# Kernel optimization log

Hardware: AMD Instinct MI355X
Metric: run time of the kernel (lower is better)

## Reference

```python
import jax, jax.numpy as jnp
from jax import lax
import numpy as np

B, N, DIM = 2, 2048, 1024
HEADS, DIM_HEAD = 16, 64
KERNELS = (0, 3, 5, 7)
GROUPS = len(KERNELS)
HPG = HEADS // GROUPS          # heads per group = 4
CG = HPG * DIM_HEAD            # channels per group for depthwise conv = 256
INNER = HEADS * DIM_HEAD       # 1024


def _alibi_slopes(n):
    # power-of-2 branch of LearnedAlibiPosBias._get_slopes (n=4 here)
    start = 2.0 ** (-(2.0 ** -(np.log2(n) - 3)))
    return np.array([start * start ** i for i in range(n)], dtype=np.float32)


def setup_inputs() -> dict:
    key = jax.random.key(0)
    ks = jax.random.split(key, 24)
    d = {}
    d['x'] = jax.random.normal(ks[0], (B, N, DIM), jnp.float32)
    d['ln_gamma'] = jnp.ones((DIM,), jnp.float32)
    d['ln_beta'] = jnp.zeros((DIM,), jnp.float32)
    d['w_qkv'] = jax.random.normal(ks[1], (3 * INNER, DIM), jnp.float32) * 0.02
    i = 2
    for p in ('q', 'k', 'v'):
        for ksz in (3, 5, 7):
            d[f'dw{p}_w{ksz}'] = jax.random.normal(ks[i], (CG, 1, ksz), jnp.float32) * 0.1; i += 1
            d[f'dw{p}_b{ksz}'] = jax.random.normal(ks[i], (CG,), jnp.float32) * 0.02; i += 1
    # learned alibi slopes, initialized to the standard ALiBi values per group
    sl = _alibi_slopes(HPG).reshape(1, HPG, 1, 1)
    d['slopes'] = jnp.asarray(np.tile(sl, (GROUPS, 1, 1, 1)))
    d['w_out'] = jax.random.normal(ks[20], (DIM, INNER), jnp.float32) * 0.02
    return d


def _dw_causal_conv(xg, w, b, ksz):
    # xg: (B, CG, N); depthwise causal conv, left pad ksz-1
    xg = jnp.pad(xg, ((0, 0), (0, 0), (ksz - 1, 0)))
    out = lax.conv_general_dilated(xg, w, (1,), 'VALID',
                                   feature_group_count=CG,
                                   dimension_numbers=('NCH', 'OIH', 'NCH'))
    return out + b[None, :, None]


def _grouped_conv(t, w3, b3, w5, b5, w7, b7):
    # t: (B, INNER, N) channels laid out head-major; group g = channels [g*CG,(g+1)*CG)
    parts = [t[:, :CG]]  # group 0: kernel_size 0 -> Identity
    for i, (w, b, ksz) in enumerate(((w3, b3, 3), (w5, b5, 5), (w7, b7, 7))):
        parts.append(_dw_causal_conv(t[:, (i + 1) * CG:(i + 2) * CG], w, b, ksz))
    out = jnp.concatenate(parts, axis=1)                      # (B, INNER, N)
    out = out.reshape(B, HEADS, DIM_HEAD, N)
    return jnp.transpose(out, (0, 1, 3, 2))                   # (B, H, N, Dh)


def _forward(x, ln_gamma, ln_beta, w_qkv,
             dwq_w3, dwq_b3, dwq_w5, dwq_b5, dwq_w7, dwq_b7,
             dwk_w3, dwk_b3, dwk_w5, dwk_b5, dwk_w7, dwk_b7,
             dwv_w3, dwv_b3, dwv_w5, dwv_b5, dwv_w7, dwv_b7,
             slopes, w_out):
    scale = DIM_HEAD ** -0.5
    mu = jnp.mean(x, axis=-1, keepdims=True)
    var = jnp.var(x, axis=-1, keepdims=True)
    h = (x - mu) * lax.rsqrt(var + 1e-5) * ln_gamma + ln_beta   # (B, N, DIM)
    qkv = jnp.einsum('bnd,ed->ben', h, w_qkv)                   # (B, 3*INNER, N)
    q, k, v = jnp.split(qkv, 3, axis=1)
    q = _grouped_conv(q, dwq_w3, dwq_b3, dwq_w5, dwq_b5, dwq_w7, dwq_b7)
    k = _grouped_conv(k, dwk_w3, dwk_b3, dwk_w5, dwk_b5, dwk_w7, dwk_b7)
    v = _grouped_conv(v, dwv_w3, dwv_b3, dwv_w5, dwv_b5, dwv_w7, dwv_b7)
    sim = jnp.einsum('bhid,bhjd->bhij', q * scale, k)           # (B, H, N, N)
    idx = jnp.arange(N)
    dist = -jnp.abs(idx[None, :] - idx[:, None]).astype(sim.dtype)  # (N, N)
    bias = slopes.reshape(HEADS, 1, 1) * dist[None]             # (H, N, N)
    sim = sim + bias[None]
    causal = idx[None, :] > idx[:, None]                        # strictly future
    sim = jnp.where(causal[None, None], -jnp.finfo(sim.dtype).max, sim)
    attn = jax.nn.softmax(sim, axis=-1)
    out = jnp.einsum('bhij,bhjd->bhid', attn, v)                # (B, H, N, Dh)
    out = jnp.transpose(out, (0, 2, 1, 3)).reshape(B, N, INNER)
    return jnp.einsum('bne,de->bnd', out, w_out)


def reference(x, ln_gamma, ln_beta, w_qkv,
              dwq_w3, dwq_b3, dwq_w5, dwq_b5, dwq_w7, dwq_b7,
              dwk_w3, dwk_b3, dwk_w5, dwk_b5, dwk_w7, dwk_b7,
              dwv_w3, dwv_b3, dwv_w5, dwv_b5, dwv_w7, dwv_b7,
              slopes, w_out):
    return _forward(x, ln_gamma, ln_beta, w_qkv,
                    dwq_w3, dwq_b3, dwq_w5, dwq_b5, dwq_w7, dwq_b7,
                    dwk_w3, dwk_b3, dwk_w5, dwk_b5, dwk_w7, dwk_b7,
                    dwv_w3, dwv_b3, dwv_w5, dwv_b5, dwv_w7, dwv_b7,
                    slopes, w_out)
```

## Files before the change

### kernel.cpp

```cpp
#include <hip/hip_runtime.h>
#include <hip/hip_bf16.h>
#include <stdint.h>

typedef __bf16 bf8 __attribute__((ext_vector_type(8)));
typedef float  f4  __attribute__((ext_vector_type(4)));

constexpr int BATCH  = 2;
constexpr int SEQ    = 2048;
constexpr int DMODEL = 1024;
constexpr int NH     = 16;
constexpr int DHEAD  = 64;
constexpr int E3     = 3072;

static __device__ __forceinline__ f4 mfma16(bf8 a, bf8 b, f4 c){
  return __builtin_amdgcn_mfma_f32_16x16x32_bf16(a, b, c, 0, 0, 0);
}
static __device__ __forceinline__ uint32_t pack2(float a, float b){
  union { __bf16 h[2]; uint32_t u; } p;
  p.h[0] = (__bf16)a; p.h[1] = (__bf16)b;
  return p.u;
}
typedef const __attribute__((address_space(1))) uint32_t g_u32;
typedef __attribute__((address_space(3))) uint32_t l_u32;
static __device__ __forceinline__ void glds16(const __bf16* g, __bf16* l){
  __builtin_amdgcn_global_load_lds((g_u32*)g, (l_u32*)l, 16, 0, 0);
}

__global__ __launch_bounds__(256) void prep_kernel(const float* __restrict__ x,
                                                   const float* __restrict__ gam,
                                                   const float* __restrict__ bet,
                                                   __bf16* __restrict__ h,
                                                   const float* __restrict__ wq,
                                                   __bf16* __restrict__ wqb){
  int bid = blockIdx.x;
  int tid = threadIdx.x;
  if(bid >= BATCH*SEQ){
    int i = ((bid - BATCH*SEQ) * 256 + tid) * 4;
    float4 v = *(const float4*)(wq + i);
    __bf16 o[4] = {(__bf16)v.x, (__bf16)v.y, (__bf16)v.z, (__bf16)v.w};
    *(uint2*)(wqb + i) = *(const uint2*)o;
    return;
  }
  int row = bid;
  const float* xr = x + (size_t)row * DMODEL;
  float4 v = *(const float4*)(xr + tid*4);
  float s = v.x + v.y + v.z + v.w;
  float ss = v.x*v.x + v.y*v.y + v.z*v.z + v.w*v.w;
#pragma unroll
  for(int m=1;m<64;m<<=1){ s += __shfl_xor(s, m); ss += __shfl_xor(ss, m); }
  __shared__ float sm[8];
  int wid = tid >> 6;
  if((tid & 63) == 0){ sm[wid] = s; sm[4+wid] = ss; }
  __syncthreads();
  s  = sm[0]+sm[1]+sm[2]+sm[3];
  ss = sm[4]+sm[5]+sm[6]+sm[7];
  float mu  = s * (1.f/DMODEL);
  float var = ss * (1.f/DMODEL) - mu*mu;
  float r = rsqrtf(var + 1e-5f);
  float4 g = *(const float4*)(gam + tid*4);
  float4 bb = *(const float4*)(bet + tid*4);
  __bf16 o[4] = { (__bf16)((v.x-mu)*r*g.x + bb.x), (__bf16)((v.y-mu)*r*g.y + bb.y),
                  (__bf16)((v.z-mu)*r*g.z + bb.z), (__bf16)((v.w-mu)*r*g.w + bb.w) };
  *(uint2*)(h + (size_t)row*DMODEL + tid*4) = *(uint2*)o;
}

template<typename CT>
__global__ __launch_bounds__(256) void gemm_nt(const __bf16* __restrict__ A,
                                               const __bf16* __restrict__ Bm,
                                               CT* __restrict__ C,
                                               int M, int Ncols, int K){
  __shared__ __align__(16) __bf16 smem[4*128*32];
  __bf16* As0 = smem;
  __bf16* Bs0 = smem + 2*128*32;
  int m0 = blockIdx.y * 128, n0 = blockIdx.x * 128;
  int tid = threadIdx.x;
  int lane = tid & 63, wid = tid >> 6;
  int quad = lane >> 4, l15 = lane & 15;
  int wm = (wid >> 1) * 64, wn = (wid & 1) * 64;
  f4 acc[4][4] = {};
  int r0 = wid*32 + (lane >> 2);
  int cofs = (lane & 3) * 8;
  const __bf16* ag = A  + (size_t)(m0 + r0) * K + cofs;
  const __bf16* bg = Bm + (size_t)(n0 + r0) * K + cofs;
  const int d0 = (wid*32)*32, d1 = (wid*32+16)*32;
  const size_t rowskip = (size_t)16 * K;
  glds16(ag,           As0 + d0);
  glds16(ag + rowskip, As0 + d1);
  glds16(bg,           Bs0 + d0);
  glds16(bg + rowskip, Bs0 + d1);
  __syncthreads();
  int cur = 0;
  for(int k0 = 0; k0 < K; k0 += 32){
    int k1 = k0 + 32;
    if(k1 < K){
      int nb = cur ^ 1;
      glds16(ag + k1,           As0 + nb*128*32 + d0);
      glds16(ag + rowskip + k1, As0 + nb*128*32 + d1);
      glds16(bg + k1,           Bs0 + nb*128*32 + d0);
      glds16(bg + rowskip + k1, Bs0 + nb*128*32 + d1);
    }
    const __bf16* AsC = As0 + cur*128*32;
    const __bf16* BsC = Bs0 + cur*128*32;
    bf8 af[4], bfr[4];
#pragma unroll
    for(int i=0;i<4;i++){
      af[i]  = *(const bf8*)&AsC[(wm + i*16 + l15)*32 + quad*8];
      bfr[i] = *(const bf8*)&BsC[(wn + i*16 + l15)*32 + quad*8];
    }
#pragma unroll
    for(int mi=0;mi<4;mi++)
#pragma unroll
      for(int ni=0;ni<4;ni++)
        acc[mi][ni] = mfma16(af[mi], bfr[ni], acc[mi][ni]);
    __syncthreads();
    cur ^= 1;
  }
  if constexpr (sizeof(CT) == 2){
    __bf16* scr = smem;
    uint32_t* sp = (uint32_t*)smem;
#pragma unroll
    for(int qq=0; qq<4; qq++){
      __syncthreads();
      if((wid>>1) == (qq>>1)){
        int mi0 = (qq & 1) * 2;
#pragma unroll
        for(int mm=0; mm<2; mm++){
          int mi = mi0 + mm;
#pragma unroll
          for(int ni=0; ni<4; ni++)
#pragma unroll
            for(int r=0; r<4; r++){
              int lr = (mi - mi0)*16 + quad*4 + r;
              scr[lr*136 + wn + ni*16 + l15] = (__bf16)acc[mi][ni][r];
            }
        }
      }
      __syncthreads();
#pragma unroll
      for(int it=0; it<2; it++){
        int idx = it*256 + tid;
        int row = idx >> 4;
        int ck  = idx & 15;
        uint4 v = { sp[row*68 + ck*4 + 0], sp[row*68 + ck*4 + 1],
                    sp[row*68 + ck*4 + 2], sp[row*68 + ck*4 + 3] };
        *(uint4*)(C + (size_t)(m0 + qq*32 + row)*Ncols + n0 + ck*8) = v;
      }
    }
  } else {
    float* scr = (float*)smem;
#pragma unroll
    for(int qq=0; qq<4; qq++){
      __syncthreads();
      if((wid>>1) == (qq>>1)){
        int mi0 = (qq & 1) * 2;
#pragma unroll
        for(int mm=0; mm<2; mm++){
          int mi = mi0 + mm;
#pragma unroll
          for(int ni=0; ni<4; ni++)
#pragma unroll
            for(int r=0; r<4; r++){
              int lr = (mi - mi0)*16 + quad*4 + r;
              scr[lr*136 + wn + ni*16 + l15] = acc[mi][ni][r];
            }
        }
      }
      __syncthreads();
#pragma unroll
      for(int it=0; it<4; it++){
        int idx = it*256 + tid;
        int row = idx >> 5;
        int ck  = idx & 31;
        float4 v = { scr[row*136 + ck*4 + 0], scr[row*136 + ck*4 + 1],
                     scr[row*136 + ck*4 + 2], scr[row*136 + ck*4 + 3] };
        *(float4*)(C + (size_t)(m0 + qq*32 + row)*Ncols + n0 + ck*4) = v;
      }
    }
  }
}

__global__ __launch_bounds__(256) void conv_kernel(const __bf16* __restrict__ qkv,
    __bf16* __restrict__ qo, __bf16* __restrict__ ko, __bf16* __restrict__ vt,
    const float* qw3,const float* qb3,const float* qw5,const float* qb5,const float* qw7,const float* qb7,
    const float* kw3,const float* kb3,const float* kw5,const float* kb5,const float* kw7,const float* kb7,
    const float* vw3,const float* vb3,const float* vw5,const float* vb5,const float* vw7,const float* vb7){
  __shared__ __align__(16) __bf16 tile[72*256];
  int nc = blockIdx.x;
  int ec = blockIdx.y;
  int b  = blockIdx.z;
  int tid = threadIdx.x;
  int n0 = nc * 64;
  {
    int rrow = tid >> 5;
    int ccol = (tid & 31) * 8;
    const __bf16* src = qkv + (size_t)b*SEQ*E3 + ec*256 + ccol;
#pragma unroll
    for(int p=0;p<9;p++){
      int row = p*8 + rrow;
      int n = n0 - 8 + row;
      uint4 v = {0u,0u,0u,0u};
      if(n >= 0) v = *(const uint4*)(src + (size_t)n*E3);
      *(uint4*)&tile[row*256 + ccol] = v;
    }
  }
  __syncthreads();
  int e = ec*256 + tid;
  int p  = e >> 10;
  int c  = e & 1023;
  int g  = c >> 8;
  int cg = c & 255;
  int hh = c >> 6;
  int dh = c & 63;
  const float* W[9]  = {qw3,qw5,qw7,kw3,kw5,kw7,vw3,vw5,vw7};
  const float* Bp[9] = {qb3,qb5,qb7,kb3,kb5,kb7,vb3,vb5,vb7};
  int ksz = (g==0)?0:((g==1)?3:((g==2)?5:7));
  float w[7] = {0,0,0,0,0,0,0};
  float bias = 0.f;
  if(g > 0){
    const float* wp = W[p*3 + g - 1];
    const float* bp = Bp[p*3 + g - 1];
    for(int t=0;t<ksz;t++) w[t] = wp[cg*ksz + t];
    bias = bp[cg];
  }
  float xh[6];
#pragma unroll
  for(int i=0;i<6;i++) xh[i] = (float)tile[(2+i)*256 + tid];
  if(p == 2){
    uint32_t vout[32];
#pragma unroll
    for(int blk=0; blk<8; blk++){
      __bf16 tmp[8];
#pragma unroll
      for(int u=0;u<8;u++){
        int dn = blk*8 + u;
        float cur = (float)tile[(8+dn)*256 + tid];
        float o;
        if(ksz == 0)      o = cur;
        else if(ksz == 3) o = w[0]*xh[4] + w[1]*xh[5] + w[2]*cur + bias;
        else if(ksz == 5) o = w[0]*xh[2] + w[1]*xh[3] + w[2]*xh[4] + w[3]*xh[5] + w[4]*cur + bias;
        else              o = w[0]*xh[0] + w[1]*xh[1] + w[2]*xh[2] + w[3]*xh[3] + w[4]*xh[4] + w[5]*xh[5] + w[6]*cur + bias;
        xh[0]=xh[1]; xh[1]=xh[2]; xh[2]=xh[3]; xh[3]=xh[4]; xh[4]=xh[5]; xh[5]=cur;
        tmp[u] = (__bf16)o;
      }
#pragma unroll
      for(int j=0;j<4;j++) vout[blk*4 + j] = ((const uint32_t*)tmp)[j];
    }
    __syncthreads();
    uint32_t* ot = (uint32_t*)tile;
#pragma unroll
    for(int j=0;j<32;j++) ot[tid*33 + j] = vout[j];
    __syncthreads();
#pragma unroll
    for(int it=0; it<8; it++){
      int idx = it*256 + tid;
      int ch  = idx >> 3;
      int ncq = idx & 7;
      uint32_t a0 = ot[ch*33 + ncq*4 + 0];
      uint32_t a1 = ot[ch*33 + ncq*4 + 1];
      uint32_t a2 = ot[ch*33 + ncq*4 + 2];
      uint32_t a3 = ot[ch*33 + ncq*4 + 3];
      uint4 val = {a0, a1, a2, a3};
      int hh2 = (ec & 3)*4 + (ch >> 6);
      int dh2 = ch & 63;
      *(uint4*)(vt + ((size_t)((b*NH + hh2)*DHEAD + dh2))*SEQ + n0 + ncq*8) = val;
    }
  } else {
    __bf16* outp = (p==0) ? qo : ko;
    __bf16* op = outp + ((size_t)(b*NH + hh)*SEQ)*DHEAD + dh;
#pragma unroll 4
    for(int dn=0; dn<64; dn++){
      float cur = (float)tile[(8+dn)*256 + tid];
      float o;
      if(ksz == 0)      o = cur;
      else if(ksz == 3) o = w[0]*xh[4] + w[1]*xh[5] + w[2]*cur + bias;
      else if(ksz == 5) o = w[0]*xh[2] + w[1]*xh[3] + w[2]*xh[4] + w[3]*xh[5] + w[4]*cur + bias;
      else              o = w[0]*xh[0] + w[1]*xh[1] + w[2]*xh[2] + w[3]*xh[3] + w[4]*xh[4] + w[5]*xh[5] + w[6]*cur + bias;
      xh[0]=xh[1]; xh[1]=xh[2]; xh[2]=xh[3]; xh[3]=xh[4]; xh[4]=xh[5]; xh[5]=cur;
      op[(size_t)(n0+dn)*DHEAD] = (__bf16)o;
    }
  }
}

__global__ __launch_bounds__(256, 2) void attn_kernel(const __bf16* __restrict__ Qin,
                                                      const __bf16* __restrict__ Kin,
                                                      const __bf16* __restrict__ Vtin,
                                                      const float* __restrict__ slopes,
                                                      __bf16* __restrict__ Oout,
                                                      const float* __restrict__ wsrc,
                                                      __bf16* __restrict__ wdst){
  __shared__ __align__(16) __bf16 Ks[2][128*64];
  __shared__ __align__(16) __bf16 Vts[2][64*128];
  __shared__ __align__(16) __bf16 Ps[4][16*72];
  __shared__ float Al[4][16];
  int bid = blockIdx.x;
  int tid = threadIdx.x;
  if(bid >= 512){
    int i = ((bid - 512) * 256 + tid) * 4;
    float4 v = *(const float4*)(wsrc + i);
    __bf16 o[4] = {(__bf16)v.x, (__bf16)v.y, (__bf16)v.z, (__bf16)v.w};
    *(uint2*)(wdst + i) = *(const uint2*)o;
    return;
  }
  int pr = bid >> 5;
  int by = (bid & 7) + ((bid >> 3) & 3) * 8;
  int b  = by >> 4, hh = by & 15;
  int lane = tid & 63, w = tid >> 6;
  int quad = lane >> 4, l15 = lane & 15;
  const __bf16* qb  = Qin  + (size_t)by * SEQ * DHEAD;
  const __bf16* kb  = Kin  + (size_t)by * SEQ * DHEAD;
  const __bf16* vtb = Vtin + (size_t)by * DHEAD * SEQ;
  const float L2E = 1.4426950408889634f;
  float slope = slopes[hh];
  const float c1 = 0.125f * L2E;
  float c2 = slope * L2E;
  float c2_64 = c2 * 64.f;
  float cjb[16];
#pragma unroll
  for(int jt=0;jt<4;jt++)
#pragma unroll
    for(int r=0;r<4;r++)
      cjb[jt*4+r] = c2 * (float)(jt*16 + quad*4 + r);

  int sxq0 = ((quad     ^ (l15 & 7)) << 3);
  int sxq1 = (((quad+4) ^ (l15 & 7)) << 3);

  const __bf16* ksrc = kb + (size_t)(lane>>3)*DHEAD + ((lane&7) ^ ((lane>>3)&7))*8;
  const __bf16* vsrc[4];
#pragma unroll
  for(int u=0;u<4;u++){
    int g = w*4 + u;
    int vrow = g*4 + (lane>>4);
    vsrc[u] = vtb + (size_t)vrow*SEQ + (((lane&15) ^ (vrow&15)) * 8);
  }

  for(int ph=0; ph<2; ph++){
    int qi = ph ? (31 - pr) : pr;
    int q0 = qi * 64;
    int nst = (qi >> 1) + 1;
    int i0 = q0 + w*16;
    int i  = i0 + l15;
    bf8 aq0 = *(const bf8*)(qb + (size_t)i*DHEAD + quad*8);
    bf8 aq1 = *(const bf8*)(qb + (size_t)i*DHEAD + 32 + quad*8);
    f4 oacc[4] = {};
    float l_ = 0.f;
#pragma unroll
    for(int u=0;u<4;u++){
      int g = w*4 + u;
      glds16(ksrc + (size_t)g*8*DHEAD, &Ks[0][g*512]);
      glds16(vsrc[u],                  &Vts[0][g*512]);
    }
    __syncthreads();
    int cur = 0;
    for(int t=0; t<nst; t++){
      int j0 = t*128;
      bool pf = (t+1) < nst;
      if(pf){
        int nb = cur ^ 1;
#pragma unroll
        for(int u=0;u<4;u++){
          int g = w*4 + u;
          glds16(ksrc + (size_t)((t+1)*128 + g*8)*DHEAD, &Ks[nb][g*512]);
          glds16(vsrc[u] + (t+1)*128,                    &Vts[nb][g*512]);
        }
      }
      const __bf16* KsC  = Ks[cur];
      const __bf16* VtsC = Vts[cur];
      f4 s[8] = {};
      __builtin_amdgcn_s_setprio(1);
#pragma unroll
      for(int jt=0;jt<8;jt++){
        bf8 ak0 = *(const bf8*)&KsC[(jt*16+l15)*64 + sxq0];
        bf8 ak1 = *(const bf8*)&KsC[(jt*16+l15)*64 + sxq1];
        s[jt] = mfma16(ak0, aq0, s[jt]);
        s[jt] = mfma16(ak1, aq1, s[jt]);
      }
      __builtin_amdgcn_s_setprio(0);
      float lsum = 0.f;
      bool masked = (t == nst-1);
      float cdi = c2 * (float)(i - j0) + 8.0f;
#pragma unroll
      for(int h=0;h<2;h++){
        bf8 bv[2][4];
#pragma unroll
        for(int jj=0;jj<2;jj++){
          int jk = h*2 + jj;
#pragma unroll
          for(int nd=0;nd<4;nd++)
            bv[jj][nd] = *(const bf8*)&VtsC[(nd*16+l15)*128 + (((jk*4+quad) ^ l15) << 3)];
        }
        float sv[4][4];
        if(!masked){
#pragma unroll
          for(int jl=0;jl<4;jl++){
            int jt = h*4 + jl;
#pragma unroll
            for(int r=0;r<4;r++)
              sv[jl][r] = fmaf(s[jt][r], c1, cjb[jl*4+r] - cdi + (h ? c2_64 : 0.f));
          }
        } else {
#pragma unroll
          for(int jl=0;jl<4;jl++){
            int jt = h*4 + jl;
#pragma unroll
            for(int r=0;r<4;r++){
              int j = j0 + jt*16 + quad*4 + r;
              int d = i - j;
              float val = fmaf(s[jt][r], c1, -fmaf(c2, (float)d, 8.0f));
              sv[jl][r] = (d < 0) ? -1e30f : val;
            }
          }
        }
#pragma unroll
        for(int jl=0;jl<4;jl++){
          float p0 = __builtin_amdgcn_exp2f(sv[jl][0]);
          float p1 = __builtin_amdgcn_exp2f(sv[jl][1]);
          float p2 = __builtin_amdgcn_exp2f(sv[jl][2]);
          float p3 = __builtin_amdgcn_exp2f(sv[jl][3]);
          lsum += (p0+p1)+(p2+p3);
          uint2 pk = { pack2(p0,p1), pack2(p2,p3) };
          *(uint2*)&Ps[w][l15*72 + jl*16 + quad*4] = pk;
        }
        __builtin_amdgcn_s_setprio(1);
#pragma unroll
        for(int jj=0;jj<2;jj++){
          bf8 ap = *(const bf8*)&Ps[w][l15*72 + jj*32 + quad*8];
#pragma unroll
          for(int nd=0;nd<4;nd++)
            oacc[nd] = mfma16(ap, bv[jj][nd], oacc[nd]);
        }
        __builtin_amdgcn_s_setprio(0);
      }
      lsum += __shfl_xor(lsum, 16);
      lsum += __shfl_xor(lsum, 32);
      l_ += lsum;
      __syncthreads();
      cur ^= 1;
    }
    if(quad == 0) Al[w][l15] = 1.0f / l_;
    f4 linv = *(const f4*)&Al[w][quad*4];
#pragma unroll
    for(int nd=0;nd<4;nd++)
#pragma unroll
      for(int r=0;r<4;r++){
        int io = i0 + quad*4 + r;
        Oout[((size_t)(b*SEQ + io))*DMODEL + hh*64 + nd*16 + l15] =
            (__bf16)(oacc[nd][r] * linv[r]);
      }
    if(ph == 0) __syncthreads();
  }
}

extern "C" void kernel_launch(void* const* d_in, const int* in_sizes, int n_in,
                              void* d_out, int out_size, void* d_ws, size_t ws_size,
                              hipStream_t stream){
  const float* x      = (const float*)d_in[0];
  const float* gam    = (const float*)d_in[1];
  const float* bet    = (const float*)d_in[2];
  const float* w_qkv  = (const float*)d_in[3];
  const float* slopes = (const float*)d_in[22];
  const float* w_out  = (const float*)d_in[23];
  float* out = (float*)d_out;

  char* ws = (char*)d_ws;
  __bf16* h       = (__bf16*)(ws);
  __bf16* qpost   = (__bf16*)(ws);
  __bf16* qkv     = (__bf16*)(ws + ((size_t)8  << 20));
  __bf16* att     = (__bf16*)(ws + ((size_t)8  << 20));
  __bf16* wout_bf = (__bf16*)(ws + ((size_t)24 << 20));
  __bf16* wqkv_bf = (__bf16*)(ws + ((size_t)32 << 20));
  __bf16* kpost   = (__bf16*)(ws + ((size_t)32 << 20));
  __bf16* vtp     = (__bf16*)(ws + ((size_t)40 << 20));

  constexpr int NQKV = 3 * DMODEL * DMODEL;

  prep_kernel<<<BATCH*SEQ + NQKV/4/256, 256, 0, stream>>>(x, gam, bet, h, w_qkv, wqkv_bf);
  gemm_nt<__bf16><<<dim3(E3/128, (BATCH*SEQ)/128), 256, 0, stream>>>(
      h, wqkv_bf, qkv, BATCH*SEQ, E3, DMODEL);
  conv_kernel<<<dim3(32, 12, BATCH), 256, 0, stream>>>(qkv, qpost, kpost, vtp,
    (const float*)d_in[4],(const float*)d_in[5],(const float*)d_in[6],(const float*)d_in[7],
    (const float*)d_in[8],(const float*)d_in[9],
    (const float*)d_in[10],(const float*)d_in[11],(const float*)d_in[12],(const float*)d_in[13],
    (const float*)d_in[14],(const float*)d_in[15],
    (const float*)d_in[16],(const float*)d_in[17],(const float*)d_in[18],(const float*)d_in[19],
    (const float*)d_in[20],(const float*)d_in[21]);
  attn_kernel<<<dim3(1536), 256, 0, stream>>>(qpost, kpost, vtp, slopes, att,
                                              w_out, wout_bf);
  gemm_nt<float><<<dim3(DMODEL/128, (BATCH*SEQ)/128), 256, 0, stream>>>(
      att, wout_bf, out, BATCH*SEQ, DMODEL, DMODEL);
}
```

Before: 235.5 us.

## Split attention into one q-tile per block with 64-wide KV tiles

The attention kernel now gives each block a single 64-row query tile, processed longest first, instead of pairing a short and a long tile inside one block. The grid grows from 512 to 1024 attention blocks. KV tiles shrink from 128 to 64 columns, which halves shared memory and raises launch bounds to 3 blocks per CU for better occupancy and finer causal load balance. In exchange there are more loop iterations and barriers per key, and blocks now finish unevenly rather than being balanced by the pairing.

```diff
diff --git a/kernel.cpp b/kernel.cpp
--- a/kernel.cpp
+++ b/kernel.cpp
@@ -281,27 +281,27 @@
   }
 }
 
-__global__ __launch_bounds__(256, 2) void attn_kernel(const __bf16* __restrict__ Qin,
+__global__ __launch_bounds__(256, 3) void attn_kernel(const __bf16* __restrict__ Qin,
                                                       const __bf16* __restrict__ Kin,
                                                       const __bf16* __restrict__ Vtin,
                                                       const float* __restrict__ slopes,
                                                       __bf16* __restrict__ Oout,
                                                       const float* __restrict__ wsrc,
                                                       __bf16* __restrict__ wdst){
-  __shared__ __align__(16) __bf16 Ks[2][128*64];
-  __shared__ __align__(16) __bf16 Vts[2][64*128];
+  __shared__ __align__(16) __bf16 Ks[2][64*64];
+  __shared__ __align__(16) __bf16 Vts[2][64*64];
   __shared__ __align__(16) __bf16 Ps[4][16*72];
   __shared__ float Al[4][16];
   int bid = blockIdx.x;
   int tid = threadIdx.x;
-  if(bid >= 512){
-    int i = ((bid - 512) * 256 + tid) * 4;
+  if(bid >= 1024){
+    int i = ((bid - 1024) * 256 + tid) * 4;
     float4 v = *(const float4*)(wsrc + i);
     __bf16 o[4] = {(__bf16)v.x, (__bf16)v.y, (__bf16)v.z, (__bf16)v.w};
     *(uint2*)(wdst + i) = *(const uint2*)o;
     return;
   }
-  int pr = bid >> 5;
+  int qi = 31 - (bid >> 5);
   int by = (bid & 7) + ((bid >> 3) & 3) * 8;
   int b  = by >> 4, hh = by & 15;
   int lane = tid & 63, w = tid >> 6;
@@ -313,7 +313,6 @@
   float slope = slopes[hh];
   const float c1 = 0.125f * L2E;
   float c2 = slope * L2E;
-  float c2_64 = c2 * 64.f;
   float cjb[16];
 #pragma unroll
   for(int jt=0;jt<4;jt++)
@@ -324,130 +323,113 @@
   int sxq0 = ((quad     ^ (l15 & 7)) << 3);
   int sxq1 = (((quad+4) ^ (l15 & 7)) << 3);
 
-  const __bf16* ksrc = kb + (size_t)(lane>>3)*DHEAD + ((lane&7) ^ ((lane>>3)&7))*8;
-  const __bf16* vsrc[4];
-#pragma unroll
-  for(int u=0;u<4;u++){
-    int g = w*4 + u;
-    int vrow = g*4 + (lane>>4);
-    vsrc[u] = vtb + (size_t)vrow*SEQ + (((lane&15) ^ (vrow&15)) * 8);
-  }
-
-  for(int ph=0; ph<2; ph++){
-    int qi = ph ? (31 - pr) : pr;
-    int q0 = qi * 64;
-    int nst = (qi >> 1) + 1;
-    int i0 = q0 + w*16;
-    int i  = i0 + l15;
-    bf8 aq0 = *(const bf8*)(qb + (size_t)i*DHEAD + quad*8);
-    bf8 aq1 = *(const bf8*)(qb + (size_t)i*DHEAD + 32 + quad*8);
-    f4 oacc[4] = {};
-    float l_ = 0.f;
-#pragma unroll
-    for(int u=0;u<4;u++){
-      int g = w*4 + u;
-      glds16(ksrc + (size_t)g*8*DHEAD, &Ks[0][g*512]);
-      glds16(vsrc[u],                  &Vts[0][g*512]);
-    }
+  int r8 = lane >> 3;
+  int c8 = lane & 7;
+  int sw = (c8 ^ r8) * 8;
+  const __bf16* ksrc = kb  + (size_t)r8*DHEAD + sw;
+  const __bf16* vsrc = vtb + (size_t)r8*SEQ  + sw;
+  int g0 = w*2, g1 = w*2 + 1;
+  const size_t kg0o = (size_t)g0*8*DHEAD, kg1o = (size_t)g1*8*DHEAD;
+  const size_t vg0o = (size_t)g0*8*SEQ,   vg1o = (size_t)g1*8*SEQ;
+
+  int q0 = qi * 64;
+  int nst = qi + 1;
+  int i0 = q0 + w*16;
+  int i  = i0 + l15;
+  bf8 aq0 = *(const bf8*)(qb + (size_t)i*DHEAD + quad*8);
+  bf8 aq1 = *(const bf8*)(qb + (size_t)i*DHEAD + 32 + quad*8);
+  f4 oacc[4] = {};
+  float l_ = 0.f;
+  glds16(ksrc + kg0o, &Ks[0][g0*512]);
+  glds16(ksrc + kg1o, &Ks[0][g1*512]);
+  glds16(vsrc + vg0o, &Vts[0][g0*512]);
+  glds16(vsrc + vg1o, &Vts[0][g1*512]);
+  __syncthreads();
+  int cur = 0;
+  for(int t=0; t<nst; t++){
+    int j0 = t*64;
+    bool pf = (t+1) < nst;
+    if(pf){
+      int nb = cur ^ 1;
+      size_t off = (size_t)(t+1)*64;
+      glds16(ksrc + off*DHEAD + kg0o, &Ks[nb][g0*512]);
+      glds16(ksrc + off*DHEAD + kg1o, &Ks[nb][g1*512]);
+      glds16(vsrc + vg0o + off,       &Vts[nb][g0*512]);
+      glds16(vsrc + vg1o + off,       &Vts[nb][g1*512]);
+    }
+    const __bf16* KsC  = Ks[cur];
+    const __bf16* VtsC = Vts[cur];
+    f4 s[4] = {};
+    __builtin_amdgcn_s_setprio(1);
+#pragma unroll
+    for(int jt=0;jt<4;jt++){
+      bf8 ak0 = *(const bf8*)&KsC[(jt*16+l15)*64 + sxq0];
+      bf8 ak1 = *(const bf8*)&KsC[(jt*16+l15)*64 + sxq1];
+      s[jt] = mfma16(ak0, aq0, s[jt]);
+      s[jt] = mfma16(ak1, aq1, s[jt]);
+    }
+    __builtin_amdgcn_s_setprio(0);
+    bf8 bv[2][4];
+#pragma unroll
+    for(int jk=0;jk<2;jk++)
+#pragma unroll
+      for(int nd=0;nd<4;nd++)
+        bv[jk][nd] = *(const bf8*)&VtsC[(nd*16+l15)*64 + (((jk*4+quad) ^ (l15&7)) << 3)];
+    float sv[4][4];
+    if(t < nst-1){
+      float cdi = c2 * (float)(i - j0) + 8.0f;
+#pragma unroll
+      for(int jt=0;jt<4;jt++)
+#pragma unroll
+        for(int r=0;r<4;r++)
+          sv[jt][r] = fmaf(s[jt][r], c1, cjb[jt*4+r] - cdi);
+    } else {
+#pragma unroll
+      for(int jt=0;jt<4;jt++)
+#pragma unroll
+        for(int r=0;r<4;r++){
+          int j = j0 + jt*16 + quad*4 + r;
+          int d = i - j;
+          float val = fmaf(s[jt][r], c1, -fmaf(c2, (float)d, 8.0f));
+          sv[jt][r] = (d < 0) ? -1e30f : val;
+        }
+    }
+    float lsum = 0.f;
+#pragma unroll
+    for(int jt=0;jt<4;jt++){
+      float p0 = __builtin_amdgcn_exp2f(sv[jt][0]);
+      float p1 = __builtin_amdgcn_exp2f(sv[jt][1]);
+      float p2 = __builtin_amdgcn_exp2f(sv[jt][2]);
+      float p3 = __builtin_amdgcn_exp2f(sv[jt][3]);
+      lsum += (p0+p1)+(p2+p3);
+      uint2 pk = { pack2(p0,p1), pack2(p2,p3) };
+      *(uint2*)&Ps[w][l15*72 + jt*16 + quad*4] = pk;
+    }
+    lsum += __shfl_xor(lsum, 16);
+    lsum += __shfl_xor(lsum, 32);
+    l_ += lsum;
+    __builtin_amdgcn_s_setprio(1);
+#pragma unroll
+    for(int jk=0;jk<2;jk++){
+      bf8 ap = *(const bf8*)&Ps[w][l15*72 + jk*32 + quad*8];
+#pragma unroll
+      for(int nd=0;nd<4;nd++)
+        oacc[nd] = mfma16(ap, bv[jk][nd], oacc[nd]);
+    }
+    __builtin_amdgcn_s_setprio(0);
     __syncthreads();
-    int cur = 0;
-    for(int t=0; t<nst; t++){
-      int j0 = t*128;
-      bool pf = (t+1) < nst;
-      if(pf){
-        int nb = cur ^ 1;
-#pragma unroll
-        for(int u=0;u<4;u++){
-          int g = w*4 + u;
-          glds16(ksrc + (size_t)((t+1)*128 + g*8)*DHEAD, &Ks[nb][g*512]);
-          glds16(vsrc[u] + (t+1)*128,                    &Vts[nb][g*512]);
-        }
-      }
-      const __bf16* KsC  = Ks[cur];
-      const __bf16* VtsC = Vts[cur];
-      f4 s[8] = {};
-      __builtin_amdgcn_s_setprio(1);
-#pragma unroll
-      for(int jt=0;jt<8;jt++){
-        bf8 ak0 = *(const bf8*)&KsC[(jt*16+l15)*64 + sxq0];
-        bf8 ak1 = *(const bf8*)&KsC[(jt*16+l15)*64 + sxq1];
-        s[jt] = mfma16(ak0, aq0, s[jt]);
-        s[jt] = mfma16(ak1, aq1, s[jt]);
-      }
-      __builtin_amdgcn_s_setprio(0);
-      float lsum = 0.f;
-      bool masked = (t == nst-1);
-      float cdi = c2 * (float)(i - j0) + 8.0f;
-#pragma unroll
-      for(int h=0;h<2;h++){
-        bf8 bv[2][4];
-#pragma unroll
-        for(int jj=0;jj<2;jj++){
-          int jk = h*2 + jj;
-#pragma unroll
-          for(int nd=0;nd<4;nd++)
-            bv[jj][nd] = *(const bf8*)&VtsC[(nd*16+l15)*128 + (((jk*4+quad) ^ l15) << 3)];
-        }
-        float sv[4][4];
-        if(!masked){
-#pragma unroll
-          for(int jl=0;jl<4;jl++){
-            int jt = h*4 + jl;
-#pragma unroll
-            for(int r=0;r<4;r++)
-              sv[jl][r] = fmaf(s[jt][r], c1, cjb[jl*4+r] - cdi + (h ? c2_64 : 0.f));
-          }
-        } else {
-#pragma unroll
-          for(int jl=0;jl<4;jl++){
-            int jt = h*4 + jl;
-#pragma unroll
-            for(int r=0;r<4;r++){
-              int j = j0 + jt*16 + quad*4 + r;
-              int d = i - j;
-              float val = fmaf(s[jt][r], c1, -fmaf(c2, (float)d, 8.0f));
-              sv[jl][r] = (d < 0) ? -1e30f : val;
-            }
-          }
-        }
-#pragma unroll
-        for(int jl=0;jl<4;jl++){
-          float p0 = __builtin_amdgcn_exp2f(sv[jl][0]);
-          float p1 = __builtin_amdgcn_exp2f(sv[jl][1]);
-          float p2 = __builtin_amdgcn_exp2f(sv[jl][2]);
-          float p3 = __builtin_amdgcn_exp2f(sv[jl][3]);
-          lsum += (p0+p1)+(p2+p3);
-          uint2 pk = { pack2(p0,p1), pack2(p2,p3) };
-          *(uint2*)&Ps[w][l15*72 + jl*16 + quad*4] = pk;
-        }
-        __builtin_amdgcn_s_setprio(1);
-#pragma unroll
-        for(int jj=0;jj<2;jj++){
-          bf8 ap = *(const bf8*)&Ps[w][l15*72 + jj*32 + quad*8];
-#pragma unroll
-          for(int nd=0;nd<4;nd++)
-            oacc[nd] = mfma16(ap, bv[jj][nd], oacc[nd]);
-        }
-        __builtin_amdgcn_s_setprio(0);
-      }
-      lsum += __shfl_xor(lsum, 16);
-      lsum += __shfl_xor(lsum, 32);
-      l_ += lsum;
-      __syncthreads();
-      cur ^= 1;
-    }
-    if(quad == 0) Al[w][l15] = 1.0f / l_;
-    f4 linv = *(const f4*)&Al[w][quad*4];
-#pragma unroll
-    for(int nd=0;nd<4;nd++)
-#pragma unroll
-      for(int r=0;r<4;r++){
-        int io = i0 + quad*4 + r;
-        Oout[((size_t)(b*SEQ + io))*DMODEL + hh*64 + nd*16 + l15] =
-            (__bf16)(oacc[nd][r] * linv[r]);
-      }
-    if(ph == 0) __syncthreads();
-  }
+    cur ^= 1;
+  }
+  if(quad == 0) Al[w][l15] = 1.0f / l_;
+  f4 linv = *(const f4*)&Al[w][quad*4];
+#pragma unroll
+  for(int nd=0;nd<4;nd++)
+#pragma unroll
+    for(int r=0;r<4;r++){
+      int io = i0 + quad*4 + r;
+      Oout[((size_t)(b*SEQ + io))*DMODEL + hh*64 + nd*16 + l15] =
+          (__bf16)(oacc[nd][r] * linv[r]);
+    }
 }
 
 extern "C" void kernel_launch(void* const* d_in, const int* in_sizes, int n_in,
@@ -483,7 +465,7 @@
     (const float*)d_in[14],(const float*)d_in[15],
     (const float*)d_in[16],(const float*)d_in[17],(const float*)d_in[18],(const float*)d_in[19],
     (const float*)d_in[20],(const float*)d_in[21]);
-  attn_kernel<<<dim3(1536), 256, 0, stream>>>(qpost, kpost, vtp, slopes, att,
+  attn_kernel<<<dim3(2048), 256, 0, stream>>>(qpost, kpost, vtp, slopes, att,
                                               w_out, wout_bf);
   gemm_nt<float><<<dim3(DMODEL/128, (BATCH*SEQ)/128), 256, 0, stream>>>(
       att, wout_bf, out, BATCH*SEQ, DMODEL, DMODEL);
```

Measured after the change: 235.9 us. About the same (+0.2%).
